# Performance work log

Hardware: AMD Instinct MI355X
Metric: run time of the kernel (lower is better)

The kernel has to match this reference:

```python
import jax, jax.numpy as jnp
import numpy as np

NB_STEPS = 7  # scaling-and-squaring steps (int_steps)


def _warp3d(vol, flow):
    """Trilinear warp: sample vol at (identity grid + flow), edge-clamped.

    vol:  (D, H, W, C) float
    flow: (D, H, W, 3) float displacement in voxel units (ij indexing)
    """
    D, H, W, C = vol.shape
    shp = (D, H, W)
    mesh = jnp.meshgrid(
        jnp.arange(D, dtype=flow.dtype),
        jnp.arange(H, dtype=flow.dtype),
        jnp.arange(W, dtype=flow.dtype),
        indexing='ij',
    )
    i0, i1, w = [], [], []
    for d, s in enumerate(shp):
        loc = jnp.clip(mesh[d] + flow[..., d], 0.0, s - 1)  # clamp = nearest fill
        f = jnp.floor(loc)
        lo = f.astype(jnp.int32)
        i0.append(lo)
        i1.append(jnp.minimum(lo + 1, s - 1))
        w.append(loc - f)
    flat = vol.reshape(-1, C)

    def gather(ii, jj, kk):
        idx = (ii * H + jj) * W + kk
        return flat[idx.reshape(-1)].reshape(D, H, W, C)

    out = jnp.zeros_like(vol)
    for bi in (0, 1):
        ii = i1[0] if bi else i0[0]
        wi = w[0] if bi else 1.0 - w[0]
        for bj in (0, 1):
            jj = i1[1] if bj else i0[1]
            wj = w[1] if bj else 1.0 - w[1]
            for bk in (0, 1):
                kk = i1[2] if bk else i0[2]
                wk = w[2] if bk else 1.0 - w[2]
                out = out + (wi * wj * wk)[..., None] * gather(ii, jj, kk)
    return out


def _integrate_ss(v):
    """Scaling-and-squaring integration of a stationary field (D,H,W,3)."""
    v = v / (2.0 ** NB_STEPS)
    for _ in range(NB_STEPS):
        v = v + _warp3d(v, v)
    return v


def setup_inputs() -> dict:
    key = jax.random.key(0)
    vec = jax.random.normal(key, (1, 160, 192, 160, 3), dtype=jnp.float32)
    return {"vec": vec}


def reference(vec):
    # vec: (B, D, H, W, 3) batched stationary velocity field
    return jax.vmap(_integrate_ss)(vec)
```

## Files before the change

kernel.cpp:

```cpp
#include <hip/hip_runtime.h>

#define D_DIM 160
#define H_DIM 192
#define W_DIM 160
#define NVOX (D_DIM * H_DIM * W_DIM)

typedef _Float16 half_t;
typedef __attribute__((ext_vector_type(4))) _Float16 H4;
typedef __attribute__((ext_vector_type(8))) _Float16 H8;

struct F3 {
    float x, y, z;
};

__device__ __forceinline__ int swz_bid(int bid, int nwg) {
    int chunk = nwg >> 3;
    return (bid & 7) * chunk + (bid >> 3);
}

__global__ __launch_bounds__(256) void scale_to_h(const float4* __restrict__ in,
                                                  H4* __restrict__ out, int n) {
    int i = blockIdx.x * blockDim.x + threadIdx.x;
    if (i >= n) return;
    float4 a = in[3 * i + 0];
    float4 b = in[3 * i + 1];
    float4 c = in[3 * i + 2];
    const float s = 0.0078125f;
    H4 o0 = {(half_t)(a.x * s), (half_t)(a.y * s), (half_t)(a.z * s), (half_t)0.f};
    H4 o1 = {(half_t)(a.w * s), (half_t)(b.x * s), (half_t)(b.y * s), (half_t)0.f};
    H4 o2 = {(half_t)(b.z * s), (half_t)(b.w * s), (half_t)(c.x * s), (half_t)0.f};
    H4 o3 = {(half_t)(c.y * s), (half_t)(c.z * s), (half_t)(c.w * s), (half_t)0.f};
    out[4 * i + 0] = o0;
    out[4 * i + 1] = o1;
    out[4 * i + 2] = o2;
    out[4 * i + 3] = o3;
}

template <int MODE>
__global__ __launch_bounds__(256) void warp_h(const H4* __restrict__ v,
                                              void* __restrict__ outp) {
    int wg = swz_bid(blockIdx.x, gridDim.x);
    int idx = wg * 256 + (int)threadIdx.x;

    int w = idx % W_DIM;
    int t = idx / W_DIM;
    int h = t % H_DIM;
    int d = t / H_DIM;

    H4 f = v[idx];
    float flow_d = (float)f.x;
    float flow_h = (float)f.y;
    float flow_w = (float)f.z;

    float ld = fminf(fmaxf((float)d + flow_d, 0.0f), (float)(D_DIM - 1));
    float lh = fminf(fmaxf((float)h + flow_h, 0.0f), (float)(H_DIM - 1));
    float lw = fminf(fmaxf((float)w + flow_w, 0.0f), (float)(W_DIM - 1));

    float fd = floorf(ld), fh = floorf(lh), fw = floorf(lw);
    int d0 = (int)fd, h0 = (int)fh, w0 = (int)fw;
    int d1 = min(d0 + 1, D_DIM - 1);
    int h1 = min(h0 + 1, H_DIM - 1);

    float wd = ld - fd, wh = lh - fh, ww = lw - fw;
    float od = 1.0f - wd, oh = 1.0f - wh, ow = 1.0f - ww;

    int r00 = (d0 * H_DIM + h0) * W_DIM;
    int r01 = (d0 * H_DIM + h1) * W_DIM;
    int r10 = (d1 * H_DIM + h0) * W_DIM;
    int r11 = (d1 * H_DIM + h1) * W_DIM;

    int b = min(w0, W_DIM - 2);
    bool hi_edge = (w0 == W_DIM - 1);

    float acc0 = 0.0f, acc1 = 0.0f, acc2 = 0.0f;
#define CORNER_PAIR(ROW, WTLO, WTHI)                                           \
    {                                                                          \
        H8 pr = *reinterpret_cast<const H8*>(v + (ROW) + b);                   \
        float l0 = hi_edge ? (float)pr[4] : (float)pr[0];                      \
        float l1 = hi_edge ? (float)pr[5] : (float)pr[1];                      \
        float l2 = hi_edge ? (float)pr[6] : (float)pr[2];                      \
        acc0 = fmaf(WTLO, l0, acc0);                                           \
        acc1 = fmaf(WTLO, l1, acc1);                                           \
        acc2 = fmaf(WTLO, l2, acc2);                                           \
        acc0 = fmaf(WTHI, (float)pr[4], acc0);                                 \
        acc1 = fmaf(WTHI, (float)pr[5], acc1);                                 \
        acc2 = fmaf(WTHI, (float)pr[6], acc2);                                 \
    }
    CORNER_PAIR(r00, od * oh * ow, od * oh * ww);
    CORNER_PAIR(r01, od * wh * ow, od * wh * ww);
    CORNER_PAIR(r10, wd * oh * ow, wd * oh * ww);
    CORNER_PAIR(r11, wd * wh * ow, wd * wh * ww);
#undef CORNER_PAIR

    float r0 = flow_d + acc0;
    float r1 = flow_h + acc1;
    float r2 = flow_w + acc2;

    if (MODE == 1) {
        H4 o = {(half_t)r0, (half_t)r1, (half_t)r2, (half_t)0.f};
        reinterpret_cast<H4*>(outp)[idx] = o;
    } else {
        F3 o;
        o.x = r0;
        o.y = r1;
        o.z = r2;
        reinterpret_cast<F3*>(outp)[idx] = o;
    }
}

extern "C" void kernel_launch(void* const* d_in, const int* in_sizes, int n_in,
                              void* d_out, int out_size, void* d_ws, size_t ws_size,
                              hipStream_t stream) {
    const float* vec = (const float*)d_in[0];
    H4* W = (H4*)d_ws;
    H4* Q = (H4*)d_out;

    int grid = NVOX / 256;

    scale_to_h<<<(NVOX / 4 + 255) / 256, 256, 0, stream>>>(
        (const float4*)vec, W, NVOX / 4);

    warp_h<1><<<grid, 256, 0, stream>>>(W, Q);
    warp_h<1><<<grid, 256, 0, stream>>>(Q, W);
    warp_h<1><<<grid, 256, 0, stream>>>(W, Q);
    warp_h<1><<<grid, 256, 0, stream>>>(Q, W);
    warp_h<1><<<grid, 256, 0, stream>>>(W, Q);
    warp_h<1><<<grid, 256, 0, stream>>>(Q, W);
    warp_h<2><<<grid, 256, 0, stream>>>(W, d_out);
}
```

Measured before the change: 194.7 us.

## Process two voxels per thread, simplify edge weights, alternate block order

Each thread now handles two adjacent W voxels. It loads both flows with a single 16-byte read and writes both outputs with one wider store, which halves the grid. The edge-case select is folded into precomputed weights (owe/wwe), so the per-corner selects go away and fewer multiplies are needed. Alternate launches reverse the per-XCD block order so that data written last by the previous kernel may still be in cache. The cost is more registers per thread and fewer waves in flight.

Result: no change. 192.1 us (-1.3%).

```diff
diff --git a/kernel.cpp b/kernel.cpp
--- a/kernel.cpp
+++ b/kernel.cpp
@@ -12,11 +12,6 @@
 struct F3 {
     float x, y, z;
 };
-
-__device__ __forceinline__ int swz_bid(int bid, int nwg) {
-    int chunk = nwg >> 3;
-    return (bid & 7) * chunk + (bid >> 3);
-}
 
 __global__ __launch_bounds__(256) void scale_to_h(const float4* __restrict__ in,
                                                   H4* __restrict__ out, int n) {
@@ -36,25 +31,12 @@
     out[4 * i + 3] = o3;
 }
 
-template <int MODE>
-__global__ __launch_bounds__(256) void warp_h(const H4* __restrict__ v,
-                                              void* __restrict__ outp) {
-    int wg = swz_bid(blockIdx.x, gridDim.x);
-    int idx = wg * 256 + (int)threadIdx.x;
-
-    int w = idx % W_DIM;
-    int t = idx / W_DIM;
-    int h = t % H_DIM;
-    int d = t / H_DIM;
-
-    H4 f = v[idx];
-    float flow_d = (float)f.x;
-    float flow_h = (float)f.y;
-    float flow_w = (float)f.z;
-
-    float ld = fminf(fmaxf((float)d + flow_d, 0.0f), (float)(D_DIM - 1));
-    float lh = fminf(fmaxf((float)h + flow_h, 0.0f), (float)(H_DIM - 1));
-    float lw = fminf(fmaxf((float)w + flow_w, 0.0f), (float)(W_DIM - 1));
+__device__ __forceinline__ void warp_voxel(const H4* __restrict__ v, int d, int h,
+                                           int w, float fx, float fy, float fz,
+                                           float& r0, float& r1, float& r2) {
+    float ld = fminf(fmaxf((float)d + fx, 0.0f), (float)(D_DIM - 1));
+    float lh = fminf(fmaxf((float)h + fy, 0.0f), (float)(H_DIM - 1));
+    float lw = fminf(fmaxf((float)w + fz, 0.0f), (float)(W_DIM - 1));
 
     float fd = floorf(ld), fh = floorf(lh), fw = floorf(lw);
     int d0 = (int)fd, h0 = (int)fh, w0 = (int)fw;
@@ -64,47 +46,69 @@
     float wd = ld - fd, wh = lh - fh, ww = lw - fw;
     float od = 1.0f - wd, oh = 1.0f - wh, ow = 1.0f - ww;
 
-    int r00 = (d0 * H_DIM + h0) * W_DIM;
-    int r01 = (d0 * H_DIM + h1) * W_DIM;
-    int r10 = (d1 * H_DIM + h0) * W_DIM;
-    int r11 = (d1 * H_DIM + h1) * W_DIM;
+    bool hi_edge = (w0 == W_DIM - 1);
+    int b = min(w0, W_DIM - 2);
+    float owe = hi_edge ? 0.0f : ow;
+    float wwe = hi_edge ? ow : ww;
 
-    int b = min(w0, W_DIM - 2);
-    bool hi_edge = (w0 == W_DIM - 1);
+    int r00 = (d0 * H_DIM + h0) * W_DIM + b;
+    int r01 = (d0 * H_DIM + h1) * W_DIM + b;
+    int r10 = (d1 * H_DIM + h0) * W_DIM + b;
+    int r11 = (d1 * H_DIM + h1) * W_DIM + b;
 
     float acc0 = 0.0f, acc1 = 0.0f, acc2 = 0.0f;
-#define CORNER_PAIR(ROW, WTLO, WTHI)                                           \
-    {                                                                          \
-        H8 pr = *reinterpret_cast<const H8*>(v + (ROW) + b);                   \
-        float l0 = hi_edge ? (float)pr[4] : (float)pr[0];                      \
-        float l1 = hi_edge ? (float)pr[5] : (float)pr[1];                      \
-        float l2 = hi_edge ? (float)pr[6] : (float)pr[2];                      \
-        acc0 = fmaf(WTLO, l0, acc0);                                           \
-        acc1 = fmaf(WTLO, l1, acc1);                                           \
-        acc2 = fmaf(WTLO, l2, acc2);                                           \
-        acc0 = fmaf(WTHI, (float)pr[4], acc0);                                 \
-        acc1 = fmaf(WTHI, (float)pr[5], acc1);                                 \
-        acc2 = fmaf(WTHI, (float)pr[6], acc2);                                 \
+#define CORNER_PAIR(ROW, FAC)                                   \
+    {                                                           \
+        H8 pr = *reinterpret_cast<const H8*>(v + (ROW));        \
+        float wlo = (FAC)*owe, whi = (FAC)*wwe;                 \
+        acc0 = fmaf(wlo, (float)pr[0], acc0);                   \
+        acc1 = fmaf(wlo, (float)pr[1], acc1);                   \
+        acc2 = fmaf(wlo, (float)pr[2], acc2);                   \
+        acc0 = fmaf(whi, (float)pr[4], acc0);                   \
+        acc1 = fmaf(whi, (float)pr[5], acc1);                   \
+        acc2 = fmaf(whi, (float)pr[6], acc2);                   \
     }
-    CORNER_PAIR(r00, od * oh * ow, od * oh * ww);
-    CORNER_PAIR(r01, od * wh * ow, od * wh * ww);
-    CORNER_PAIR(r10, wd * oh * ow, wd * oh * ww);
-    CORNER_PAIR(r11, wd * wh * ow, wd * wh * ww);
+    CORNER_PAIR(r00, od * oh);
+    CORNER_PAIR(r01, od * wh);
+    CORNER_PAIR(r10, wd * oh);
+    CORNER_PAIR(r11, wd * wh);
 #undef CORNER_PAIR
 
-    float r0 = flow_d + acc0;
-    float r1 = flow_h + acc1;
-    float r2 = flow_w + acc2;
+    r0 = fx + acc0;
+    r1 = fy + acc1;
+    r2 = fz + acc2;
+}
+
+template <int MODE, bool REV>
+__global__ __launch_bounds__(256) void warp_h(const H4* __restrict__ v,
+                                              void* __restrict__ outp) {
+    int chunk = gridDim.x >> 3;
+    int xcd = blockIdx.x & 7;
+    int local = blockIdx.x >> 3;
+    if (REV) local = chunk - 1 - local;
+    int wg = xcd * chunk + local;
+
+    int base = wg * 512 + (int)threadIdx.x * 2;
+
+    int w = base % W_DIM;
+    int t = base / W_DIM;
+    int h = t % H_DIM;
+    int d = t / H_DIM;
+
+    H8 fl = *reinterpret_cast<const H8*>(v + base);
+
+    float a0, a1, a2, b0, b1, b2;
+    warp_voxel(v, d, h, w, (float)fl[0], (float)fl[1], (float)fl[2], a0, a1, a2);
+    warp_voxel(v, d, h, w + 1, (float)fl[4], (float)fl[5], (float)fl[6], b0, b1, b2);
 
     if (MODE == 1) {
-        H4 o = {(half_t)r0, (half_t)r1, (half_t)r2, (half_t)0.f};
-        reinterpret_cast<H4*>(outp)[idx] = o;
+        H8 o = {(half_t)a0, (half_t)a1, (half_t)a2, (half_t)0.f,
+                (half_t)b0, (half_t)b1, (half_t)b2, (half_t)0.f};
+        *reinterpret_cast<H8*>(reinterpret_cast<H4*>(outp) + base) = o;
     } else {
-        F3 o;
-        o.x = r0;
-        o.y = r1;
-        o.z = r2;
-        reinterpret_cast<F3*>(outp)[idx] = o;
+        F3* o = reinterpret_cast<F3*>(outp);
+        o[base] = F3{a0, a1, a2};
+        o[base + 1] = F3{b0, b1, b2};
     }
 }
 
@@ -115,16 +119,16 @@
     H4* W = (H4*)d_ws;
     H4* Q = (H4*)d_out;
 
-    int grid = NVOX / 256;
-
     scale_to_h<<<(NVOX / 4 + 255) / 256, 256, 0, stream>>>(
         (const float4*)vec, W, NVOX / 4);
 
-    warp_h<1><<<grid, 256, 0, stream>>>(W, Q);
-    warp_h<1><<<grid, 256, 0, stream>>>(Q, W);
-    warp_h<1><<<grid, 256, 0, stream>>>(W, Q);
-    warp_h<1><<<grid, 256, 0, stream>>>(Q, W);
-    warp_h<1><<<grid, 256, 0, stream>>>(W, Q);
-    warp_h<1><<<grid, 256, 0, stream>>>(Q, W);
-    warp_h<2><<<grid, 256, 0, stream>>>(W, d_out);
+    int grid = NVOX / 512;
+
+    warp_h<1, false><<<grid, 256, 0, stream>>>(W, Q);
+    warp_h<1, true><<<grid, 256, 0, stream>>>(Q, W);
+    warp_h<1, false><<<grid, 256, 0, stream>>>(W, Q);
+    warp_h<1, true><<<grid, 256, 0, stream>>>(Q, W);
+    warp_h<1, false><<<grid, 256, 0, stream>>>(W, Q);
+    warp_h<1, true><<<grid, 256, 0, stream>>>(Q, W);
+    warp_h<2, false><<<grid, 256, 0, stream>>>(W, d_out);
 }
```
